# Optimization experiments

Hardware: AMD Instinct MI355X
Metric: run time of the kernel (lower is better)

The kernel has to match this reference:

```python
import jax, jax.numpy as jnp
import numpy as np

B, H, N = 128, 512, 1024

def setup_inputs() -> dict:
    key = jax.random.key(0)
    ks = jax.random.split(key, 9)
    s = 1.0 / np.sqrt(H)
    return {
        "mc_hidden": jax.random.normal(ks[0], (B, H), jnp.float32),
        "sn_hidden": jax.random.normal(ks[1], (B, H, N), jnp.float32),
        "attn_W": jax.random.normal(ks[2], (H, 2 * H), jnp.float32) * s,
        "attn_v": jax.random.normal(ks[3], (H,), jnp.float32) * s,
        "ptr_v": jax.random.normal(ks[4], (H,), jnp.float32) * s,
        "fc1_W": jax.random.normal(ks[5], (H, 2 * H), jnp.float32) * s,
        "fc1_b": jax.random.normal(ks[6], (H,), jnp.float32) * s,
        "fc2_W": jax.random.normal(ks[7], (H, H), jnp.float32) * s,
        "fc2_b": jax.random.normal(ks[8], (H,), jnp.float32) * s,
    }


def reference(mc_hidden, sn_hidden, attn_W, attn_v, ptr_v, fc1_W, fc1_b, fc2_W, fc2_b):
    # ---- Attention (Bahdanau-style additive scoring) ----
    # hidden: (B, 2H, N) = cat(sn_hidden, mc expanded along N) on dim 1
    mc_exp = jnp.broadcast_to(mc_hidden[:, :, None], sn_hidden.shape)  # (B,H,N)
    hidden = jnp.concatenate((sn_hidden, mc_exp), axis=1)              # (B,2H,N)
    # W @ hidden -> (B,H,N); v @ tanh(.) -> (B,N)
    scores = jnp.einsum('h,bhn->bn', attn_v,
                        jnp.tanh(jnp.einsum('hk,bkn->bhn', attn_W, hidden)))
    attns = jax.nn.softmax(scores, axis=-1)                            # (B,N)
    # ---- Context + pointer scoring ----
    context = jnp.einsum('bn,bhn->bh', attns, sn_hidden)               # (B,H)
    x = jnp.concatenate((mc_hidden, context), axis=1)                  # (B,2H)
    out = jax.nn.relu(x @ fc1_W.T + fc1_b)                             # (B,H)
    out = jax.nn.relu(out @ fc2_W.T + fc2_b)                           # (B,H)
    probs = jnp.einsum('h,bhn->bn', ptr_v,
                       jnp.tanh(sn_hidden + out[:, :, None]))          # (B,N)
    return probs
```

## Files before the change

### kernel.cpp

```cpp
#include <hip/hip_runtime.h>
#include <hip/hip_bf16.h>

#define Bn 128
#define Hd 512
#define Nn 1024

typedef __attribute__((ext_vector_type(8))) short short8;
typedef __attribute__((ext_vector_type(4))) float f32x4;

#define GLOAD_LDS16(gptr, lptr)                                                     \
    __builtin_amdgcn_global_load_lds(                                               \
        (const __attribute__((address_space(1))) void*)(gptr),                      \
        (__attribute__((address_space(3))) void*)(lptr), 16, 0, 0)

__device__ __forceinline__ unsigned pack_bf2(float a, float b) {
    __hip_bfloat162 h = __float22bfloat162_rn(float2{a, b});
    unsigned u;
    __builtin_memcpy(&u, &h, 4);
    return u;
}

__device__ __forceinline__ float wave_sum(float v) {
    v += __shfl_xor(v, 32);
    v += __shfl_xor(v, 16);
    v += __shfl_xor(v, 8);
    v += __shfl_xor(v, 4);
    v += __shfl_xor(v, 2);
    v += __shfl_xor(v, 1);
    return v;
}

__device__ __forceinline__ float tanh_fast(float x) {
    float e = __expf(2.0f * x);
    return 1.0f - 2.0f * __builtin_amdgcn_rcpf(e + 1.0f);
}

__global__ void pre_kernel(const float* __restrict__ attn_W,
                           const float* __restrict__ mc,
                           unsigned short* __restrict__ Wb,
                           float* __restrict__ mc_term) {
    if (blockIdx.x < 128) {
        int idx = (blockIdx.x * 256 + threadIdx.x) * 8;
        int h = idx >> 9;
        int k = idx & 511;
        const float* p = attn_W + (size_t)h * 1024 + k;
        float4 v0 = *(const float4*)p;
        float4 v1 = *(const float4*)(p + 4);
        unsigned u[4] = {pack_bf2(v0.x, v0.y), pack_bf2(v0.z, v0.w),
                         pack_bf2(v1.x, v1.y), pack_bf2(v1.z, v1.w)};
        *(uint4*)(Wb + idx) = *(uint4*)u;
        return;
    }
    int wg = ((blockIdx.x - 128) * 256 + threadIdx.x) >> 6;
    int lane = threadIdx.x & 63;
    int b = wg >> 9;
    int h = wg & 511;
    const float* m = mc + b * Hd + lane * 8;
    const float* w = attn_W + (size_t)h * 1024 + 512 + lane * 8;
    float4 m0 = *(const float4*)m, m1 = *(const float4*)(m + 4);
    float4 w0 = *(const float4*)w, w1 = *(const float4*)(w + 4);
    float acc = m0.x * w0.x + m0.y * w0.y + m0.z * w0.z + m0.w * w0.w +
                m1.x * w1.x + m1.y * w1.y + m1.z * w1.z + m1.w * w1.w;
    acc = wave_sum(acc);
    if (lane == 0) mc_term[b * Hd + h] = acc;
}

__global__ __launch_bounds__(256, 2)
void attn_score_kernel(const float* __restrict__ sn,
                       const unsigned short* __restrict__ Wb,
                       const float* __restrict__ attn_v,
                       const float* __restrict__ mc_term,
                       float* __restrict__ scores_part) {
    __shared__ __align__(16) unsigned short A_lds[256 * 64];
    __shared__ __align__(16) unsigned B_kp[32 * 132];
    __shared__ float av_s[256];
    __shared__ float mct_s[256];
    __shared__ float ssum[128];

    const int bid = blockIdx.x;
    const int b = bid >> 4;
    const int mh = (bid >> 3) & 1;
    const int n0 = (bid & 7) << 7;
    const int tid = threadIdx.x;
    const int lane = tid & 63;
    const int wid = tid >> 6;
    const int quad = lane >> 4;
    const int l15 = lane & 15;

    av_s[tid] = attn_v[mh * 256 + tid];
    mct_s[tid] = mc_term[b * Hd + mh * 256 + tid];
    if (tid < 128) ssum[tid] = 0.f;

    f32x4 acc[4][8];
#pragma unroll
    for (int i = 0; i < 4; ++i)
#pragma unroll
        for (int j = 0; j < 8; ++j) {
            f32x4 z = {0.f, 0.f, 0.f, 0.f};
            acc[i][j] = z;
        }

    const int r8 = lane >> 3;
    const int csw = ((lane & 7) ^ r8) * 16;
    const char* Wg = (const char*)Wb + (size_t)(mh * 256) * 1024;
    const int key = l15 & 7;

    const int kp_l = tid >> 5;
    const int n4 = (tid & 31) * 4;
    const float* snb = sn + (size_t)b * Hd * Nn + n0 + n4;

    for (int k0 = 0; k0 < 512; k0 += 64) {
#pragma unroll
        for (int i = 0; i < 8; ++i) {
            const int row = wid * 64 + i * 8;
            GLOAD_LDS16(Wg + (size_t)(row + r8) * 1024 + k0 * 2 + csw,
                        (char*)A_lds + row * 128);
        }
#pragma unroll
        for (int j = 0; j < 4; ++j) {
            const int kp = j * 8 + kp_l;
            const float* p0 = snb + (size_t)(k0 + 2 * kp) * Nn;
            float4 f0 = *(const float4*)p0;
            float4 f1 = *(const float4*)(p0 + Nn);
            unsigned u[4];
            u[0] = pack_bf2(f0.x, f1.x);
            u[1] = pack_bf2(f0.y, f1.y);
            u[2] = pack_bf2(f0.z, f1.z);
            u[3] = pack_bf2(f0.w, f1.w);
            *(uint4*)&B_kp[kp * 132 + n4] = *(uint4*)u;
        }
        __syncthreads();
#pragma unroll
        for (int kk = 0; kk < 2; ++kk) {
            const int cb = quad + kk * 4;
            short8 bfr[8], afr[4];
#pragma unroll
            for (int nt = 0; nt < 8; ++nt) {
                const int nl = nt * 16 + l15;
                uint4 uu;
                uu.x = B_kp[(cb * 4 + 0) * 132 + nl];
                uu.y = B_kp[(cb * 4 + 1) * 132 + nl];
                uu.z = B_kp[(cb * 4 + 2) * 132 + nl];
                uu.w = B_kp[(cb * 4 + 3) * 132 + nl];
                bfr[nt] = *(short8*)&uu;
            }
#pragma unroll
            for (int mt = 0; mt < 4; ++mt) {
                const int m = wid * 64 + mt * 16 + l15;
                afr[mt] = *(const short8*)((const char*)A_lds + m * 128 + ((cb ^ key) * 16));
            }
#pragma unroll
            for (int mt = 0; mt < 4; ++mt)
#pragma unroll
                for (int nt = 0; nt < 8; ++nt)
                    acc[mt][nt] = __builtin_amdgcn_mfma_f32_16x16x32_bf16(afr[mt], bfr[nt], acc[mt][nt], 0, 0, 0);
        }
        __syncthreads();
    }

    float s[8] = {0.f, 0.f, 0.f, 0.f, 0.f, 0.f, 0.f, 0.f};
#pragma unroll
    for (int mt = 0; mt < 4; ++mt) {
        int hb = wid * 64 + mt * 16 + quad * 4;
#pragma unroll
        for (int r = 0; r < 4; ++r) {
            float av = av_s[hb + r];
            float mcv = mct_s[hb + r];
#pragma unroll
            for (int nt = 0; nt < 8; ++nt)
                s[nt] += av * tanh_fast(acc[mt][nt][r] + mcv);
        }
    }
#pragma unroll
    for (int nt = 0; nt < 8; ++nt) {
        float v = s[nt];
        v += __shfl_xor(v, 16);
        v += __shfl_xor(v, 32);
        if (lane < 16) atomicAdd(&ssum[nt * 16 + l15], v);
    }
    __syncthreads();
    if (tid < 128)
        scores_part[((size_t)mh * Bn + b) * Nn + n0 + tid] = ssum[tid];
}

__global__ void softmax_kernel(const float* __restrict__ scores_part,
                               float* __restrict__ attns) {
    const int b = blockIdx.x;
    const int tid = threadIdx.x;
    const int lane = tid & 63, wid = tid >> 6;
    __shared__ float red[4];
    const float* s0 = scores_part + (size_t)b * Nn;
    const float* s1 = scores_part + ((size_t)Bn + b) * Nn;
    float v[4];
#pragma unroll
    for (int i = 0; i < 4; ++i) {
        int idx = tid + i * 256;
        v[i] = s0[idx] + s1[idx];
    }
    float m = fmaxf(fmaxf(v[0], v[1]), fmaxf(v[2], v[3]));
#pragma unroll
    for (int off = 32; off >= 1; off >>= 1) m = fmaxf(m, __shfl_xor(m, off));
    if (lane == 0) red[wid] = m;
    __syncthreads();
    m = fmaxf(fmaxf(red[0], red[1]), fmaxf(red[2], red[3]));
    __syncthreads();
    float s = 0.f;
#pragma unroll
    for (int i = 0; i < 4; ++i) {
        v[i] = __expf(v[i] - m);
        s += v[i];
    }
    s = wave_sum(s);
    if (lane == 0) red[wid] = s;
    __syncthreads();
    s = red[0] + red[1] + red[2] + red[3];
    float inv = __builtin_amdgcn_rcpf(s);
#pragma unroll
    for (int i = 0; i < 4; ++i) attns[b * Nn + tid + i * 256] = v[i] * inv;
}

__global__ void context_kernel(const float* __restrict__ sn,
                               const float* __restrict__ attns,
                               float* __restrict__ context) {
    int b = blockIdx.x >> 3;
    int h0 = (blockIdx.x & 7) << 6;
    int t = threadIdx.x;
    __shared__ float a_s[1024];
    *(float4*)&a_s[t * 4] = *(const float4*)&attns[b * Nn + t * 4];
    __syncthreads();
    int h = h0 + (t >> 2), q = t & 3;
    const float* row = sn + ((size_t)b * Hd + h) * Nn;
    float acc = 0.f;
#pragma unroll 8
    for (int j = 0; j < 64; ++j) {
        int n = q * 4 + j * 16;
        float4 f = *(const float4*)&row[n];
        float4 a = *(const float4*)&a_s[n];
        acc += f.x * a.x + f.y * a.y + f.z * a.z + f.w * a.w;
    }
    acc += __shfl_xor(acc, 1);
    acc += __shfl_xor(acc, 2);
    if (q == 0) context[b * Hd + h] = acc;
}

__global__ void fc1_kernel(const float* __restrict__ mc,
                           const float* __restrict__ ctx,
                           const float* __restrict__ fc1_W,
                           const float* __restrict__ fc1_b,
                           float* __restrict__ out1) {
    int wg = (blockIdx.x * blockDim.x + threadIdx.x) >> 6;
    int lane = threadIdx.x & 63;
    int b = wg >> 9, h = wg & 511;
    const float* wr = fc1_W + (size_t)h * 1024;
    float acc = 0.f;
    {
        float4 w0 = *(const float4*)(wr + lane * 8);
        float4 w1 = *(const float4*)(wr + lane * 8 + 4);
        float4 x0 = *(const float4*)(mc + b * Hd + lane * 8);
        float4 x1 = *(const float4*)(mc + b * Hd + lane * 8 + 4);
        acc += w0.x * x0.x + w0.y * x0.y + w0.z * x0.z + w0.w * x0.w;
        acc += w1.x * x1.x + w1.y * x1.y + w1.z * x1.z + w1.w * x1.w;
    }
    {
        float4 w0 = *(const float4*)(wr + 512 + lane * 8);
        float4 w1 = *(const float4*)(wr + 512 + lane * 8 + 4);
        float4 x0 = *(const float4*)(ctx + b * Hd + lane * 8);
        float4 x1 = *(const float4*)(ctx + b * Hd + lane * 8 + 4);
        acc += w0.x * x0.x + w0.y * x0.y + w0.z * x0.z + w0.w * x0.w;
        acc += w1.x * x1.x + w1.y * x1.y + w1.z * x1.z + w1.w * x1.w;
    }
    acc = wave_sum(acc);
    if (lane == 0) out1[b * Hd + h] = fmaxf(acc + fc1_b[h], 0.f);
}

__global__ void fc2_kernel(const float* __restrict__ out1,
                           const float* __restrict__ fc2_W,
                           const float* __restrict__ fc2_b,
                           float* __restrict__ out2) {
    int wg = (blockIdx.x * blockDim.x + threadIdx.x) >> 6;
    int lane = threadIdx.x & 63;
    int b = wg >> 9, h = wg & 511;
    const float* wr = fc2_W + (size_t)h * 512 + lane * 8;
    float4 w0 = *(const float4*)wr;
    float4 w1 = *(const float4*)(wr + 4);
    float4 x0 = *(const float4*)(out1 + b * Hd + lane * 8);
    float4 x1 = *(const float4*)(out1 + b * Hd + lane * 8 + 4);
    float acc = w0.x * x0.x + w0.y * x0.y + w0.z * x0.z + w0.w * x0.w +
                w1.x * x1.x + w1.y * x1.y + w1.z * x1.z + w1.w * x1.w;
    acc = wave_sum(acc);
    if (lane == 0) out2[b * Hd + h] = fmaxf(acc + fc2_b[h], 0.f);
}

__global__ void final_kernel(const float* __restrict__ sn,
                             const float* __restrict__ ptr_v,
                             const float* __restrict__ out2,
                             float* __restrict__ probs) {
    int b = blockIdx.x >> 2;
    int n0 = (blockIdx.x & 3) << 8;
    int t = threadIdx.x;
    int w = t >> 6, l = t & 63;
    __shared__ float pv_s[512], o2_s[512];
    __shared__ float fsum[4][256];
    pv_s[t] = ptr_v[t];
    pv_s[t + 256] = ptr_v[t + 256];
    o2_s[t] = out2[b * Hd + t];
    o2_s[t + 256] = out2[b * Hd + t + 256];
    __syncthreads();
    const float* col = sn + (size_t)b * Hd * Nn + n0 + l * 4;
    float a0 = 0.f, a1 = 0.f, a2 = 0.f, a3 = 0.f;
#pragma unroll 4
    for (int j = 0; j < 128; ++j) {
        int h = w * 128 + j;
        float4 f = *(const float4*)&col[(size_t)h * Nn];
        float p = pv_s[h], o = o2_s[h];
        a0 += p * tanh_fast(f.x + o);
        a1 += p * tanh_fast(f.y + o);
        a2 += p * tanh_fast(f.z + o);
        a3 += p * tanh_fast(f.w + o);
    }
    fsum[w][l * 4 + 0] = a0;
    fsum[w][l * 4 + 1] = a1;
    fsum[w][l * 4 + 2] = a2;
    fsum[w][l * 4 + 3] = a3;
    __syncthreads();
    float r = fsum[0][t & 255] + fsum[1][t & 255] + fsum[2][t & 255] + fsum[3][t & 255];
    probs[b * Nn + n0 + (t & 255)] = r;
}

extern "C" void kernel_launch(void* const* d_in, const int* in_sizes, int n_in,
                              void* d_out, int out_size, void* d_ws, size_t ws_size,
                              hipStream_t stream) {
    const float* mc  = (const float*)d_in[0];
    const float* sn  = (const float*)d_in[1];
    const float* aW  = (const float*)d_in[2];
    const float* av  = (const float*)d_in[3];
    const float* pv  = (const float*)d_in[4];
    const float* f1W = (const float*)d_in[5];
    const float* f1b = (const float*)d_in[6];
    const float* f2W = (const float*)d_in[7];
    const float* f2b = (const float*)d_in[8];

    unsigned short* Wb = (unsigned short*)d_ws;
    float* fws         = (float*)(Wb + 512 * 512);
    float* mc_term     = fws;
    float* scores_part = mc_term + Bn * Hd;
    float* attns       = scores_part + 2 * Bn * Nn;
    float* context     = attns + Bn * Nn;
    float* out1        = context + Bn * Hd;
    float* out2        = out1 + Bn * Hd;
    float* probs       = (float*)d_out;

    pre_kernel<<<dim3(16512), dim3(256), 0, stream>>>(aW, mc, Wb, mc_term);
    attn_score_kernel<<<dim3(2048), dim3(256), 0, stream>>>(sn, Wb, av, mc_term, scores_part);
    softmax_kernel<<<dim3(128), dim3(256), 0, stream>>>(scores_part, attns);
    context_kernel<<<dim3(1024), dim3(256), 0, stream>>>(sn, attns, context);
    fc1_kernel<<<dim3(16384), dim3(256), 0, stream>>>(mc, context, f1W, f1b, out1);
    fc2_kernel<<<dim3(16384), dim3(256), 0, stream>>>(out1, f2W, f2b, out2);
    final_kernel<<<dim3(512), dim3(256), 0, stream>>>(sn, pv, out2, probs);
}
```

Baseline: 527.3 us.

## Swizzle B tile LDS layout for vector reads and fuse softmax into context

The attention-score GEMM now stages the sn tile in LDS as n-major rows of 64 bf16 k-values with an XOR swizzle, so each MFMA B fragment is one 16-byte LDS read instead of four scalar reads. Each thread now loads eight strided scalar floats along k rather than two float4s, which makes the global loads less coalesced. Separately, softmax is fused into the context kernel so the attns buffer and one launch go away. Each of the 8 blocks per batch row now recomputes the softmax, adding some redundant work.

```diff
diff --git a/kernel.cpp b/kernel.cpp
--- a/kernel.cpp
+++ b/kernel.cpp
@@ -72,7 +72,7 @@
                        const float* __restrict__ mc_term,
                        float* __restrict__ scores_part) {
     __shared__ __align__(16) unsigned short A_lds[256 * 64];
-    __shared__ __align__(16) unsigned B_kp[32 * 132];
+    __shared__ __align__(16) unsigned short B_lds[128 * 64];
     __shared__ float av_s[256];
     __shared__ float mct_s[256];
     __shared__ float ssum[128];
@@ -105,9 +105,10 @@
     const char* Wg = (const char*)Wb + (size_t)(mh * 256) * 1024;
     const int key = l15 & 7;
 
-    const int kp_l = tid >> 5;
-    const int n4 = (tid & 31) * 4;
-    const float* snb = sn + (size_t)b * Hd * Nn + n0 + n4;
+    const int cB = tid >> 5;
+    const int nbB = tid & 31;
+    const int bswz = ((cB ^ (nbB & 7)) * 16);
+    const float* snB = sn + (size_t)b * Hd * Nn + n0 + nbB + (size_t)(8 * cB) * Nn;
 
     for (int k0 = 0; k0 < 512; k0 += 64) {
 #pragma unroll
@@ -116,18 +117,18 @@
             GLOAD_LDS16(Wg + (size_t)(row + r8) * 1024 + k0 * 2 + csw,
                         (char*)A_lds + row * 128);
         }
-#pragma unroll
-        for (int j = 0; j < 4; ++j) {
-            const int kp = j * 8 + kp_l;
-            const float* p0 = snb + (size_t)(k0 + 2 * kp) * Nn;
-            float4 f0 = *(const float4*)p0;
-            float4 f1 = *(const float4*)(p0 + Nn);
-            unsigned u[4];
-            u[0] = pack_bf2(f0.x, f1.x);
-            u[1] = pack_bf2(f0.y, f1.y);
-            u[2] = pack_bf2(f0.z, f1.z);
-            u[3] = pack_bf2(f0.w, f1.w);
-            *(uint4*)&B_kp[kp * 132 + n4] = *(uint4*)u;
+        {
+            const float* pk = snB + (size_t)k0 * Nn;
+#pragma unroll
+            for (int j = 0; j < 4; ++j) {
+                const int n = nbB + 32 * j;
+                const float* p = pk + 32 * j;
+                float v0 = p[0 * Nn], v1 = p[1 * Nn], v2 = p[2 * Nn], v3 = p[3 * Nn];
+                float v4 = p[4 * Nn], v5 = p[5 * Nn], v6 = p[6 * Nn], v7 = p[7 * Nn];
+                unsigned kp[4] = {pack_bf2(v0, v1), pack_bf2(v2, v3),
+                                  pack_bf2(v4, v5), pack_bf2(v6, v7)};
+                *(uint4*)((char*)B_lds + n * 128 + bswz) = *(uint4*)kp;
+            }
         }
         __syncthreads();
 #pragma unroll
@@ -137,12 +138,7 @@
 #pragma unroll
             for (int nt = 0; nt < 8; ++nt) {
                 const int nl = nt * 16 + l15;
-                uint4 uu;
-                uu.x = B_kp[(cb * 4 + 0) * 132 + nl];
-                uu.y = B_kp[(cb * 4 + 1) * 132 + nl];
-                uu.z = B_kp[(cb * 4 + 2) * 132 + nl];
-                uu.w = B_kp[(cb * 4 + 3) * 132 + nl];
-                bfr[nt] = *(short8*)&uu;
+                bfr[nt] = *(const short8*)((const char*)B_lds + nl * 128 + ((cb ^ key) * 16));
             }
 #pragma unroll
             for (int mt = 0; mt < 4; ++mt) {
@@ -183,18 +179,22 @@
         scores_part[((size_t)mh * Bn + b) * Nn + n0 + tid] = ssum[tid];
 }
 
-__global__ void softmax_kernel(const float* __restrict__ scores_part,
-                               float* __restrict__ attns) {
-    const int b = blockIdx.x;
-    const int tid = threadIdx.x;
-    const int lane = tid & 63, wid = tid >> 6;
+__global__ void softmax_context_kernel(const float* __restrict__ sn,
+                                       const float* __restrict__ scores_part,
+                                       float* __restrict__ context) {
+    int b = blockIdx.x >> 3;
+    int h0 = (blockIdx.x & 7) << 6;
+    int t = threadIdx.x;
+    int lane = t & 63, wid = t >> 6;
     __shared__ float red[4];
+    __shared__ float a_s[1024];
+
     const float* s0 = scores_part + (size_t)b * Nn;
     const float* s1 = scores_part + ((size_t)Bn + b) * Nn;
     float v[4];
 #pragma unroll
     for (int i = 0; i < 4; ++i) {
-        int idx = tid + i * 256;
+        int idx = t + i * 256;
         v[i] = s0[idx] + s1[idx];
     }
     float m = fmaxf(fmaxf(v[0], v[1]), fmaxf(v[2], v[3]));
@@ -216,18 +216,9 @@
     s = red[0] + red[1] + red[2] + red[3];
     float inv = __builtin_amdgcn_rcpf(s);
 #pragma unroll
-    for (int i = 0; i < 4; ++i) attns[b * Nn + tid + i * 256] = v[i] * inv;
-}
-
-__global__ void context_kernel(const float* __restrict__ sn,
-                               const float* __restrict__ attns,
-                               float* __restrict__ context) {
-    int b = blockIdx.x >> 3;
-    int h0 = (blockIdx.x & 7) << 6;
-    int t = threadIdx.x;
-    __shared__ float a_s[1024];
-    *(float4*)&a_s[t * 4] = *(const float4*)&attns[b * Nn + t * 4];
-    __syncthreads();
+    for (int i = 0; i < 4; ++i) a_s[t + i * 256] = v[i] * inv;
+    __syncthreads();
+
     int h = h0 + (t >> 2), q = t & 3;
     const float* row = sn + ((size_t)b * Hd + h) * Nn;
     float acc = 0.f;
@@ -344,16 +335,14 @@
     float* fws         = (float*)(Wb + 512 * 512);
     float* mc_term     = fws;
     float* scores_part = mc_term + Bn * Hd;
-    float* attns       = scores_part + 2 * Bn * Nn;
-    float* context     = attns + Bn * Nn;
+    float* context     = scores_part + 2 * Bn * Nn;
     float* out1        = context + Bn * Hd;
     float* out2        = out1 + Bn * Hd;
     float* probs       = (float*)d_out;
 
     pre_kernel<<<dim3(16512), dim3(256), 0, stream>>>(aW, mc, Wb, mc_term);
     attn_score_kernel<<<dim3(2048), dim3(256), 0, stream>>>(sn, Wb, av, mc_term, scores_part);
-    softmax_kernel<<<dim3(128), dim3(256), 0, stream>>>(scores_part, attns);
-    context_kernel<<<dim3(1024), dim3(256), 0, stream>>>(sn, attns, context);
+    softmax_context_kernel<<<dim3(1024), dim3(256), 0, stream>>>(sn, scores_part, context);
     fc1_kernel<<<dim3(16384), dim3(256), 0, stream>>>(mc, context, f1W, f1b, out1);
     fc2_kernel<<<dim3(16384), dim3(256), 0, stream>>>(out1, f2W, f2b, out2);
     final_kernel<<<dim3(512), dim3(256), 0, stream>>>(sn, pv, out2, probs);
```

After: 524.7 us. No clear change (-0.5%).
